# Performance work log

Measured on AMD Instinct MI355X. Metric: run time of the kernel, lower is better.

Reference implementation:

```python
import jax, jax.numpy as jnp
import numpy as np

N_ITER = 100
EPS = 1e-12


def _corr(x, k):
    # x: [C,H,W], k: [kh,kw]; per-channel 'same' cross-correlation, zero padding
    C = x.shape[0]
    kern = jnp.broadcast_to(k, (C, 1) + k.shape)
    return jax.lax.conv_general_dilated(
        x[None], kern, window_strides=(1, 1), padding='SAME',
        feature_group_count=C,
        dimension_numbers=('NCHW', 'OIHW', 'NCHW'))[0]


def _corr_t(x, k):
    # adjoint of zero-padded 'same' correlation = correlation with flipped kernel
    return _corr(x, k[::-1, ::-1])


def _A(x, kernel, reg_kernels, w2):
    # A x = K^T K x + sum_i w_i^2 R_i^T R_i x
    out = _corr_t(_corr(x, kernel), kernel)
    for i in range(reg_kernels.shape[0]):  # small fixed number of reg kernels
        rk = reg_kernels[i]
        out = out + w2[i] * _corr_t(_corr(x, rk), rk)
    return out


def setup_inputs() -> dict:
    key = jax.random.key(0)
    k1, k2, k3, k4 = jax.random.split(key, 4)
    image = jax.random.uniform(k1, (3, 768, 768), dtype=jnp.float32)
    kernel = jax.random.uniform(k2, (15, 15), dtype=jnp.float32)
    kernel = kernel / jnp.sum(kernel)  # normalized blur PSF
    reg_kernels = jax.random.normal(k3, (2, 5, 5), dtype=jnp.float32)
    reg_kernel_weights = jax.random.uniform(
        k4, (2,), dtype=jnp.float32, minval=1e-6, maxval=1.0)
    return {'image': image, 'kernel': kernel, 'reg_kernels': reg_kernels,
            'reg_kernel_weights': reg_kernel_weights}


def reference(image, kernel, reg_kernels, reg_kernel_weights):
    w2 = reg_kernel_weights ** 2
    # CG init: x0 = image, b = image, solve A x = K^T b
    KTb = _corr_t(image, kernel)
    r0 = KTb - _A(image, kernel, reg_kernels, w2)
    xrp0 = jnp.stack([image, r0, r0])  # [3, C, H, W]: x, r, p

    def body(xrp, _):
        x, r, p = xrp[0], xrp[1], xrp[2]
        Ap = _A(p, kernel, reg_kernels, w2)
        rtr = jnp.sum(r * r, axis=(1, 2), keepdims=True)      # per-channel [C,1,1]
        ptAp = jnp.sum(p * Ap, axis=(1, 2), keepdims=True)
        alpha = rtr / (ptAp + EPS)
        x_new = x + alpha * p
        r_new = r - alpha * Ap
        beta = jnp.sum(r_new * r_new, axis=(1, 2), keepdims=True) / (rtr + EPS)
        p_new = r_new + beta * p
        return jnp.stack([x_new, r_new, p_new]), None

    xrp, _ = jax.lax.scan(jax.checkpoint(body), xrp0, None, length=N_ITER)
    return xrp
```

## Files before the change

### kernel.cpp

```cpp
#include <hip/hip_runtime.h>

#define EPS 1e-12f

constexpr int H = 768, W = 768, C = 3;
constexpr int HW = H * W;
constexpr int CHW = C * HW;

constexpr int NSLOT = 16;
constexpr int SSTR = 16;
constexpr int SCALSZ = NSLOT * SSTR;

constexpr int SPW = 100, SPH = 60;
constexpr int S0W = 84,  S0H = 46;
constexpr int S1W = 76,  S1H = 36;
constexpr int UBUF = SPH * SPW;

__device__ __forceinline__ float block_reduce_256(float v, float* redbuf) {
    #pragma unroll
    for (int off = 32; off > 0; off >>= 1) v += __shfl_down(v, off, 64);
    const int tid = threadIdx.x;
    if ((tid & 63) == 0) redbuf[tid >> 6] = v;
    __syncthreads();
    return redbuf[0] + redbuf[1] + redbuf[2] + redbuf[3];
}

__device__ __forceinline__ float sum_slots(const float* base, int c) {
    float s = 0.f;
    #pragma unroll
    for (int k = 0; k < NSLOT; ++k) s += base[k * SSTR + c];
    return s;
}

__global__ void tap_prep_k(const float* __restrict__ k15, const float* __restrict__ rks,
                           float* __restrict__ taps) {
    const int tid = threadIdx.x;
    if (tid < 240) {
        const int i = tid >> 4, j = tid & 15;
        taps[tid]       = (j < 15) ? k15[i * 15 + j] : 0.f;
        taps[240 + tid] = (j < 15) ? k15[(14 - i) * 15 + (14 - j)] : 0.f;
    }
    if (tid < 80) {
        const int kk = tid / 40, rem = tid % 40, i = rem >> 3, j = rem & 7;
        taps[480 + tid] = (j < 5) ? rks[kk * 25 + i * 5 + j] : 0.f;
        taps[560 + tid] = (j < 5) ? rks[kk * 25 + (4 - i) * 5 + (4 - j)] : 0.f;
    }
}

template <int MODE>
__global__ __launch_bounds__(256) void fusedA_k(
    const float* __restrict__ in, const float* __restrict__ rvec,
    const float* __restrict__ taps, const float* __restrict__ rw,
    float* __restrict__ Ap, float* __restrict__ outR,
    float* __restrict__ outP, float* __restrict__ outX,
    const float* __restrict__ bnum, const float* __restrict__ bden,
    float* __restrict__ red)
{
    __shared__ __align__(16) float ub[UBUF];
    __shared__ __align__(16) float st1[S1H * S1W];
    __shared__ __align__(16) float st2[S1H * S1W];
    __shared__ float redbuf[4];

    const float* kt   = taps;
    const float* ktf  = taps + 240;
    const float* rkt  = taps + 480;
    const float* rktf = taps + 560;

    const int c = blockIdx.z;
    const int bx = blockIdx.x * 64, by = blockIdx.y * 32;
    const int tid = threadIdx.x;
    const float* inC = in + c * HW;

    float beta = 0.f;
    if (MODE == 2) beta = sum_slots(bnum, c) / (sum_slots(bden, c) + EPS);

    for (int t = tid; t < SPH * 96; t += 256) {
        const int ly = t / 96, lx = t - ly * 96;
        const int gy = by - 14 + ly, gx = bx - 14 + lx;
        float v = 0.f;
        if ((unsigned)gy < (unsigned)H && (unsigned)gx < (unsigned)W) {
            const int g = gy * W + gx;
            v = inC[g];
            if (MODE == 2) v = rvec[c * HW + g] + beta * v;
        }
        ub[ly * SPW + lx] = v;
    }
    __syncthreads();

    const int oy = tid >> 3;
    const int ox = (tid & 7) << 3;

    {
        const int s0 = tid, s1 = tid + 256;
        const int row0 = s0 / 9, c0 = (s0 - row0 * 9) << 3;
        const int row1 = s1 / 9, c1 = (s1 - row1 * 9) << 3;
        const bool v1 = (s1 < 324);
        float b0[8], c0a[8], b1[8], c1a[8];
        #pragma unroll
        for (int k = 0; k < 8; ++k) { b0[k] = 0.f; c0a[k] = 0.f; b1[k] = 0.f; c1a[k] = 0.f; }

        float4 kb0 = *(const float4*)(rkt + 0), kb1 = *(const float4*)(rkt + 4);
        float4 kc0 = *(const float4*)(rkt + 40), kc1 = *(const float4*)(rkt + 44);
        #pragma unroll 1
        for (int i = 0; i < 5; ++i) {
            const int ip = (i < 4) ? i + 1 : 4;
            float4 nb0 = *(const float4*)(rkt + ip * 8),      nb1 = *(const float4*)(rkt + ip * 8 + 4);
            float4 nc0 = *(const float4*)(rkt + 40 + ip * 8), nc1 = *(const float4*)(rkt + 40 + ip * 8 + 4);
            float kb[8], kc[8];
            *(float4*)(kb) = kb0; *(float4*)(kb + 4) = kb1;
            *(float4*)(kc) = kc0; *(float4*)(kc + 4) = kc1;

            {
                const float* rp = ub + (row0 + 10 + i) * SPW + c0 + 8;
                float seg[16];
                #pragma unroll
                for (int q = 0; q < 4; ++q) *(float4*)(seg + 4 * q) = *(const float4*)(rp + 4 * q);
                #pragma unroll
                for (int j = 0; j < 5; ++j)
                    #pragma unroll
                    for (int k = 0; k < 8; ++k) {
                        b0[k]  = fmaf(seg[j + k + 2], kb[j], b0[k]);
                        c0a[k] = fmaf(seg[j + k + 2], kc[j], c0a[k]);
                    }
            }
            if (v1) {
                const float* rp = ub + (row1 + 10 + i) * SPW + c1 + 8;
                float seg[16];
                #pragma unroll
                for (int q = 0; q < 4; ++q) *(float4*)(seg + 4 * q) = *(const float4*)(rp + 4 * q);
                #pragma unroll
                for (int j = 0; j < 5; ++j)
                    #pragma unroll
                    for (int k = 0; k < 8; ++k) {
                        b1[k]  = fmaf(seg[j + k + 2], kb[j], b1[k]);
                        c1a[k] = fmaf(seg[j + k + 2], kc[j], c1a[k]);
                    }
            }
            kb0 = nb0; kb1 = nb1; kc0 = nc0; kc1 = nc1;
        }
        {
            const int gy = by - 2 + row0, gxb = bx - 2 + c0;
            #pragma unroll
            for (int k = 0; k < 8; ++k) {
                const bool bad = ((unsigned)gy >= (unsigned)H) || ((unsigned)(gxb + k) >= (unsigned)W);
                if (bad) { b0[k] = 0.f; c0a[k] = 0.f; }
            }
            float* o1 = st1 + row0 * S1W + c0;
            float* o2 = st2 + row0 * S1W + c0;
            *(float4*)(o1)     = make_float4(b0[0], b0[1], b0[2], b0[3]);
            *(float4*)(o1 + 4) = make_float4(b0[4], b0[5], b0[6], b0[7]);
            *(float4*)(o2)     = make_float4(c0a[0], c0a[1], c0a[2], c0a[3]);
            *(float4*)(o2 + 4) = make_float4(c0a[4], c0a[5], c0a[6], c0a[7]);
        }
        if (v1) {
            const int gy = by - 2 + row1, gxb = bx - 2 + c1;
            #pragma unroll
            for (int k = 0; k < 8; ++k) {
                const bool bad = ((unsigned)gy >= (unsigned)H) || ((unsigned)(gxb + k) >= (unsigned)W);
                if (bad) { b1[k] = 0.f; c1a[k] = 0.f; }
            }
            float* o1 = st1 + row1 * S1W + c1;
            float* o2 = st2 + row1 * S1W + c1;
            *(float4*)(o1)     = make_float4(b1[0], b1[1], b1[2], b1[3]);
            *(float4*)(o1 + 4) = make_float4(b1[4], b1[5], b1[6], b1[7]);
            *(float4*)(o2)     = make_float4(c1a[0], c1a[1], c1a[2], c1a[3]);
            *(float4*)(o2 + 4) = make_float4(c1a[4], c1a[5], c1a[6], c1a[7]);
        }
    }

    float pctr[8];
    {
        const float* ctr = ub + (oy + 14) * SPW + ox + 14;
        #pragma unroll
        for (int k = 0; k < 8; ++k) pctr[k] = ctr[k];
    }

    float vimg[8];
    if (MODE == 0) {
        #pragma unroll
        for (int k = 0; k < 8; ++k) vimg[k] = 0.f;
        #pragma unroll 1
        for (int i = 0; i < 15; ++i) {
            const float* rowp = ub + (oy + 7 + i) * SPW + ox + 4;
            float seg[28];
            #pragma unroll
            for (int q = 0; q < 7; ++q) *(float4*)(seg + 4 * q) = *(const float4*)(rowp + 4 * q);
            float kv[16];
            #pragma unroll
            for (int q = 0; q < 4; ++q) *(float4*)(kv + 4 * q) = *(const float4*)(ktf + i * 16 + 4 * q);
            #pragma unroll
            for (int j = 0; j < 15; ++j)
                #pragma unroll
                for (int k = 0; k < 8; ++k) vimg[k] = fmaf(seg[j + k + 3], kv[j], vimg[k]);
        }
    }

    const int s0 = tid, s1 = tid + 256;
    const int row0 = s0 / 10, ca0 = (s0 - row0 * 10) << 3;
    const int row1 = s1 / 10, ca1 = (s1 - row1 * 10) << 3;
    const bool av1 = (s1 < 460);
    float a0[8], a1[8];
    #pragma unroll
    for (int k = 0; k < 8; ++k) { a0[k] = 0.f; a1[k] = 0.f; }
    {
        float4 k0 = *(const float4*)(kt + 0), k1 = *(const float4*)(kt + 4);
        float4 k2 = *(const float4*)(kt + 8), k3 = *(const float4*)(kt + 12);
        #pragma unroll 1
        for (int i = 0; i < 15; ++i) {
            const int ip = (i < 14) ? i + 1 : 14;
            float4 n0 = *(const float4*)(kt + ip * 16),     n1 = *(const float4*)(kt + ip * 16 + 4);
            float4 n2 = *(const float4*)(kt + ip * 16 + 8), n3 = *(const float4*)(kt + ip * 16 + 12);
            float kv[16];
            *(float4*)(kv) = k0; *(float4*)(kv + 4) = k1;
            *(float4*)(kv + 8) = k2; *(float4*)(kv + 12) = k3;
            {
                const float* rp = ub + (row0 + i) * SPW + ca0;
                float seg[24];
                #pragma unroll
                for (int q = 0; q < 6; ++q) *(float4*)(seg + 4 * q) = *(const float4*)(rp + 4 * q);
                #pragma unroll
                for (int j = 0; j < 15; ++j)
                    #pragma unroll
                    for (int k = 0; k < 8; ++k) a0[k] = fmaf(seg[j + k], kv[j], a0[k]);
            }
            if (av1) {
                const float* rp = ub + (row1 + i) * SPW + ca1;
                float seg[24];
                #pragma unroll
                for (int q = 0; q < 6; ++q) *(float4*)(seg + 4 * q) = *(const float4*)(rp + 4 * q);
                #pragma unroll
                for (int j = 0; j < 15; ++j)
                    #pragma unroll
                    for (int k = 0; k < 8; ++k) a1[k] = fmaf(seg[j + k], kv[j], a1[k]);
            }
            k0 = n0; k1 = n1; k2 = n2; k3 = n3;
        }
    }
    {
        const int gy = by - 7 + row0, gxb = bx - 7 + ca0;
        #pragma unroll
        for (int k = 0; k < 8; ++k)
            if (((unsigned)gy >= (unsigned)H) || ((unsigned)(gxb + k) >= (unsigned)W)) a0[k] = 0.f;
    }
    if (av1) {
        const int gy = by - 7 + row1, gxb = bx - 7 + ca1;
        #pragma unroll
        for (int k = 0; k < 8; ++k)
            if (((unsigned)gy >= (unsigned)H) || ((unsigned)(gxb + k) >= (unsigned)W)) a1[k] = 0.f;
    }

    __syncthreads();

    {
        float* o = ub + row0 * S0W + ca0;
        *(float4*)(o)     = make_float4(a0[0], a0[1], a0[2], a0[3]);
        *(float4*)(o + 4) = make_float4(a0[4], a0[5], a0[6], a0[7]);
    }
    if (av1) {
        float* o = ub + row1 * S0W + ca1;
        *(float4*)(o)     = make_float4(a1[0], a1[1], a1[2], a1[3]);
        *(float4*)(o + 4) = make_float4(a1[4], a1[5], a1[6], a1[7]);
    }
    __syncthreads();

    float acc[8];
    #pragma unroll
    for (int k = 0; k < 8; ++k) acc[k] = 0.f;
    {
        float4 k0 = *(const float4*)(ktf + 0), k1 = *(const float4*)(ktf + 4);
        float4 k2 = *(const float4*)(ktf + 8), k3 = *(const float4*)(ktf + 12);
        #pragma unroll 1
        for (int i = 0; i < 15; ++i) {
            const int ip = (i < 14) ? i + 1 : 14;
            float4 n0 = *(const float4*)(ktf + ip * 16),     n1 = *(const float4*)(ktf + ip * 16 + 4);
            float4 n2 = *(const float4*)(ktf + ip * 16 + 8), n3 = *(const float4*)(ktf + ip * 16 + 12);
            float kv[16];
            *(float4*)(kv) = k0; *(float4*)(kv + 4) = k1;
            *(float4*)(kv + 8) = k2; *(float4*)(kv + 12) = k3;
            const float* rp = ub + (oy + i) * S0W + ox;
            float seg[24];
            #pragma unroll
            for (int q = 0; q < 6; ++q) *(float4*)(seg + 4 * q) = *(const float4*)(rp + 4 * q);
            #pragma unroll
            for (int j = 0; j < 15; ++j)
                #pragma unroll
                for (int k = 0; k < 8; ++k) acc[k] = fmaf(seg[j + k], kv[j], acc[k]);
            k0 = n0; k1 = n1; k2 = n2; k3 = n3;
        }
    }

    float accB[8], accC[8];
    #pragma unroll
    for (int k = 0; k < 8; ++k) { accB[k] = 0.f; accC[k] = 0.f; }
    {
        float4 kb0 = *(const float4*)(rktf + 0), kb1 = *(const float4*)(rktf + 4);
        float4 kc0 = *(const float4*)(rktf + 40), kc1 = *(const float4*)(rktf + 44);
        #pragma unroll 1
        for (int i = 0; i < 5; ++i) {
            const int ip = (i < 4) ? i + 1 : 4;
            float4 nb0 = *(const float4*)(rktf + ip * 8),      nb1 = *(const float4*)(rktf + ip * 8 + 4);
            float4 nc0 = *(const float4*)(rktf + 40 + ip * 8), nc1 = *(const float4*)(rktf + 40 + ip * 8 + 4);
            float kb[8], kc[8];
            *(float4*)(kb) = kb0; *(float4*)(kb + 4) = kb1;
            *(float4*)(kc) = kc0; *(float4*)(kc + 4) = kc1;
            const float* r1p = st1 + (oy + i) * S1W + ox;
            const float* r2p = st2 + (oy + i) * S1W + ox;
            float sA[12], sB[12];
            #pragma unroll
            for (int q = 0; q < 3; ++q) *(float4*)(sA + 4 * q) = *(const float4*)(r1p + 4 * q);
            #pragma unroll
            for (int q = 0; q < 3; ++q) *(float4*)(sB + 4 * q) = *(const float4*)(r2p + 4 * q);
            #pragma unroll
            for (int j = 0; j < 5; ++j)
                #pragma unroll
                for (int k = 0; k < 8; ++k) {
                    accB[k] = fmaf(sA[j + k], kb[j], accB[k]);
                    accC[k] = fmaf(sB[j + k], kc[j], accC[k]);
                }
            kb0 = nb0; kb1 = nb1; kc0 = nc0; kc1 = nc1;
        }
    }

    const float w0 = rw[0], w1 = rw[1];
    const float w02 = w0 * w0, w12 = w1 * w1;
    float v[8];
    #pragma unroll
    for (int k = 0; k < 8; ++k) v[k] = acc[k] + w02 * accB[k] + w12 * accC[k];

    const int g = c * HW + (by + oy) * W + bx + ox;
    float local = 0.f;
    if (MODE == 0) {
        #pragma unroll
        for (int k = 0; k < 8; ++k) v[k] = vimg[k] - v[k];
        *(float4*)(outR + g)     = make_float4(v[0], v[1], v[2], v[3]);
        *(float4*)(outR + g + 4) = make_float4(v[4], v[5], v[6], v[7]);
        *(float4*)(outP + g)     = make_float4(v[0], v[1], v[2], v[3]);
        *(float4*)(outP + g + 4) = make_float4(v[4], v[5], v[6], v[7]);
        *(float4*)(outX + g)     = make_float4(pctr[0], pctr[1], pctr[2], pctr[3]);
        *(float4*)(outX + g + 4) = make_float4(pctr[4], pctr[5], pctr[6], pctr[7]);
        #pragma unroll
        for (int k = 0; k < 8; ++k) local += v[k] * v[k];
    } else {
        *(float4*)(Ap + g)     = make_float4(v[0], v[1], v[2], v[3]);
        *(float4*)(Ap + g + 4) = make_float4(v[4], v[5], v[6], v[7]);
        #pragma unroll
        for (int k = 0; k < 8; ++k) local += pctr[k] * v[k];
        if (MODE == 2) {
            *(float4*)(outP + g)     = make_float4(pctr[0], pctr[1], pctr[2], pctr[3]);
            *(float4*)(outP + g + 4) = make_float4(pctr[4], pctr[5], pctr[6], pctr[7]);
        }
    }
    const float tot = block_reduce_256(local, redbuf);
    if (tid == 0) {
        const int bid = blockIdx.y * gridDim.x + blockIdx.x;
        atomicAdd(red + (bid & (NSLOT - 1)) * SSTR + c, tot);
    }
}

__global__ __launch_bounds__(256) void cg_update_k(
    float* __restrict__ x, float* __restrict__ r,
    const float* __restrict__ Ap, const float* __restrict__ p,
    const float* __restrict__ rtr_cur, const float* __restrict__ ptap,
    float* __restrict__ rtr_next)
{
    __shared__ float redbuf[4];
    const int c = blockIdx.z;
    const float n = sum_slots(rtr_cur, c), d = sum_slots(ptap, c);
    const float alpha = n / (d + EPS);
    const int idx = c * HW + (blockIdx.x * 256 + threadIdx.x) * 8;
    float local = 0.f;
    #pragma unroll
    for (int h = 0; h < 2; ++h) {
        const int o = idx + 4 * h;
        float4 xv = *(float4*)(x + o);
        float4 rv = *(float4*)(r + o);
        const float4 pv = *(const float4*)(p + o);
        const float4 av = *(const float4*)(Ap + o);
        xv.x = fmaf(alpha, pv.x, xv.x); rv.x = fmaf(-alpha, av.x, rv.x);
        xv.y = fmaf(alpha, pv.y, xv.y); rv.y = fmaf(-alpha, av.y, rv.y);
        xv.z = fmaf(alpha, pv.z, xv.z); rv.z = fmaf(-alpha, av.z, rv.z);
        xv.w = fmaf(alpha, pv.w, xv.w); rv.w = fmaf(-alpha, av.w, rv.w);
        *(float4*)(x + o) = xv;
        *(float4*)(r + o) = rv;
        local += rv.x * rv.x + rv.y * rv.y + rv.z * rv.z + rv.w * rv.w;
    }
    const float tot = block_reduce_256(local, redbuf);
    if (threadIdx.x == 0)
        atomicAdd(rtr_next + ((int)blockIdx.x & (NSLOT - 1)) * SSTR + c, tot);
}

__global__ __launch_bounds__(256) void p_final_k(
    const float* __restrict__ r, const float* __restrict__ p99, float* __restrict__ pout,
    const float* __restrict__ num, const float* __restrict__ den)
{
    const int c = blockIdx.z;
    const float beta = sum_slots(num, c) / (sum_slots(den, c) + EPS);
    const int idx = c * HW + (blockIdx.x * 256 + threadIdx.x) * 8;
    #pragma unroll
    for (int h = 0; h < 2; ++h) {
        const int o = idx + 4 * h;
        const float4 rv = *(const float4*)(r + o);
        const float4 pv = *(const float4*)(p99 + o);
        *(float4*)(pout + o) = make_float4(
            fmaf(beta, pv.x, rv.x), fmaf(beta, pv.y, rv.y),
            fmaf(beta, pv.z, rv.z), fmaf(beta, pv.w, rv.w));
    }
}

extern "C" void kernel_launch(void* const* d_in, const int* in_sizes, int n_in,
                              void* d_out, int out_size, void* d_ws, size_t ws_size,
                              hipStream_t stream)
{
    const float* img = (const float*)d_in[0];
    const float* k15 = (const float*)d_in[1];
    const float* rks = (const float*)d_in[2];
    const float* rw  = (const float*)d_in[3];

    float* out = (float*)d_out;
    float* xs = out;
    float* rs = out + CHW;
    float* ps = out + 2 * CHW;

    float* ws   = (float*)d_ws;
    float* buf0 = ws;
    float* Ap   = buf0 + CHW;
    float* scal = Ap + CHW;
    float* rtr2 = scal;
    float* ptap = scal + 101 * SCALSZ;
    float* taps = scal + 201 * SCALSZ;

    hipMemsetAsync(scal, 0, (size_t)(101 + 100) * SCALSZ * sizeof(float), stream);
    tap_prep_k<<<1, 256, 0, stream>>>(k15, rks, taps);

    const dim3 gc(W / 64, H / 32, C), bc(256);
    const dim3 ge(HW / 2048, 1, C);

    fusedA_k<0><<<gc, bc, 0, stream>>>(img, nullptr, taps, rw,
                                       nullptr, rs, buf0, xs,
                                       nullptr, nullptr, rtr2);

    for (int i = 0; i < 100; ++i) {
        float* pin  = (i & 1) ? buf0 : ps;
        float* pcur = (i & 1) ? ps : buf0;
        if (i == 0) {
            fusedA_k<1><<<gc, bc, 0, stream>>>(buf0, nullptr, taps, rw,
                                               Ap, nullptr, nullptr, nullptr,
                                               nullptr, nullptr, ptap);
        } else {
            fusedA_k<2><<<gc, bc, 0, stream>>>(pin, rs, taps, rw,
                                               Ap, nullptr, pcur, nullptr,
                                               rtr2 + i * SCALSZ, rtr2 + (i - 1) * SCALSZ,
                                               ptap + i * SCALSZ);
        }
        cg_update_k<<<ge, bc, 0, stream>>>(xs, rs, Ap, pcur,
                                           rtr2 + i * SCALSZ, ptap + i * SCALSZ,
                                           rtr2 + (i + 1) * SCALSZ);
    }
    p_final_k<<<ge, bc, 0, stream>>>(rs, ps, ps, rtr2 + 100 * SCALSZ, rtr2 + 99 * SCALSZ);
}
```

Baseline: 9.897 ms.

## Collapse normal-equation operator into single 29x29 stencil for interior tiles

Precomputes the composed kernel K^T K + sum w_i^2 R_i^T R_i as one 29x29 autocorrelation stencil and applies it in a new interior kernel. The interior kernel does a single pass, so it avoids staging the intermediate correlation results in shared memory. Border tiles, where zero padding makes the composed stencil wrong, still use the original two-pass fused kernel, launched on a remapped 1-D edge grid. The 29x29 stencil costs about 841 FMAs per pixel, versus fewer for separate 15x15 and 5x5 passes, so the trade is more arithmetic for less shared-memory traffic and fewer syncs, plus an extra launch per iteration.

```diff
diff --git a/kernel.cpp b/kernel.cpp
--- a/kernel.cpp
+++ b/kernel.cpp
@@ -14,6 +14,8 @@
 constexpr int S0W = 84,  S0H = 46;
 constexpr int S1W = 76,  S1H = 36;
 constexpr int UBUF = SPH * SPW;
+
+constexpr int IPW = 92, IPH = 60;
 
 __device__ __forceinline__ float block_reduce_256(float v, float* redbuf) {
     #pragma unroll
@@ -32,7 +34,7 @@
 }
 
 __global__ void tap_prep_k(const float* __restrict__ k15, const float* __restrict__ rks,
-                           float* __restrict__ taps) {
+                           const float* __restrict__ rw, float* __restrict__ taps) {
     const int tid = threadIdx.x;
     if (tid < 240) {
         const int i = tid >> 4, j = tid & 15;
@@ -44,9 +46,135 @@
         taps[480 + tid] = (j < 5) ? rks[kk * 25 + i * 5 + j] : 0.f;
         taps[560 + tid] = (j < 5) ? rks[kk * 25 + (4 - i) * 5 + (4 - j)] : 0.f;
     }
-}
-
-template <int MODE>
+    const float w20 = rw[0] * rw[0], w21 = rw[1] * rw[1];
+    for (int t = tid; t < 29 * 36; t += 256) {
+        const int uy = t / 36, ux = t - uy * 36;
+        float s = 0.f;
+        if (ux < 29) {
+            const int dy = uy - 14, dx = ux - 14;
+            for (int sy = 0; sy < 15; ++sy) {
+                const int ty = sy + dy;
+                if ((unsigned)ty >= 15u) continue;
+                for (int sx = 0; sx < 15; ++sx) {
+                    const int tx = sx + dx;
+                    if ((unsigned)tx < 15u) s += k15[sy * 15 + sx] * k15[ty * 15 + tx];
+                }
+            }
+            if (dy >= -4 && dy <= 4 && dx >= -4 && dx <= 4) {
+                float q0 = 0.f, q1 = 0.f;
+                for (int sy = 0; sy < 5; ++sy) {
+                    const int ty = sy + dy;
+                    if ((unsigned)ty >= 5u) continue;
+                    for (int sx = 0; sx < 5; ++sx) {
+                        const int tx = sx + dx;
+                        if ((unsigned)tx >= 5u) continue;
+                        q0 += rks[sy * 5 + sx] * rks[ty * 5 + tx];
+                        q1 += rks[25 + sy * 5 + sx] * rks[25 + ty * 5 + tx];
+                    }
+                }
+                s += w20 * q0 + w21 * q1;
+            }
+        }
+        taps[640 + t] = s;
+    }
+}
+
+template <bool WRITEP>
+__global__ __launch_bounds__(256) void interiorA_k(
+    const float* __restrict__ pprev, const float* __restrict__ rvec,
+    const float* __restrict__ tk,
+    float* __restrict__ Ap, float* __restrict__ outP,
+    const float* __restrict__ bnum, const float* __restrict__ bden,
+    float* __restrict__ red)
+{
+    __shared__ __align__(16) float pe[IPH * IPW];
+    __shared__ float redbuf[4];
+    const int c = blockIdx.z;
+    const int bx = 64 + blockIdx.x * 64, by = 32 + blockIdx.y * 32;
+    const int tid = threadIdx.x;
+    const float beta = sum_slots(bnum, c) / (sum_slots(bden, c) + EPS);
+    const float* pC = pprev + c * HW;
+    const float* rC = rvec + c * HW;
+    const int gy0 = by - 14, gx0 = bx - 14;
+
+    for (int t = tid; t < IPH * IPW; t += 256) {
+        const int ly = t / IPW, lx = t - ly * IPW;
+        const int g = (gy0 + ly) * W + gx0 + lx;
+        pe[t] = fmaf(beta, pC[g], rC[g]);
+    }
+    __syncthreads();
+
+    const int ox = (tid & 15) << 2;
+    const int o0 = (tid >> 4) << 1;
+
+    float a0[4], a1[4];
+    #pragma unroll
+    for (int k = 0; k < 4; ++k) { a0[k] = 0.f; a1[k] = 0.f; }
+
+    {
+        const float* rp = pe + o0 * IPW + ox;
+        float seg[32];
+        #pragma unroll
+        for (int q = 0; q < 8; ++q) *(float4*)(seg + 4 * q) = *(const float4*)(rp + 4 * q);
+        #pragma unroll
+        for (int j = 0; j < 29; ++j) {
+            const float kv = tk[j];
+            #pragma unroll
+            for (int k = 0; k < 4; ++k) a0[k] = fmaf(seg[j + k], kv, a0[k]);
+        }
+    }
+    #pragma unroll 1
+    for (int d = 1; d <= 28; ++d) {
+        const float* rp = pe + (o0 + d) * IPW + ox;
+        float seg[32];
+        #pragma unroll
+        for (int q = 0; q < 8; ++q) *(float4*)(seg + 4 * q) = *(const float4*)(rp + 4 * q);
+        const float* kr0 = tk + d * 36;
+        const float* kr1 = kr0 - 36;
+        #pragma unroll
+        for (int j = 0; j < 29; ++j) {
+            const float kv0 = kr0[j], kv1 = kr1[j];
+            #pragma unroll
+            for (int k = 0; k < 4; ++k) {
+                a0[k] = fmaf(seg[j + k], kv0, a0[k]);
+                a1[k] = fmaf(seg[j + k], kv1, a1[k]);
+            }
+        }
+    }
+    {
+        const float* rp = pe + (o0 + 29) * IPW + ox;
+        float seg[32];
+        #pragma unroll
+        for (int q = 0; q < 8; ++q) *(float4*)(seg + 4 * q) = *(const float4*)(rp + 4 * q);
+        const float* kr1 = tk + 28 * 36;
+        #pragma unroll
+        for (int j = 0; j < 29; ++j) {
+            const float kv = kr1[j];
+            #pragma unroll
+            for (int k = 0; k < 4; ++k) a1[k] = fmaf(seg[j + k], kv, a1[k]);
+        }
+    }
+
+    const int gbase = c * HW + (by + o0) * W + bx + ox;
+    const float* c0p = pe + (o0 + 14) * IPW + ox + 14;
+    const float* c1p = c0p + IPW;
+    *(float4*)(Ap + gbase)     = make_float4(a0[0], a0[1], a0[2], a0[3]);
+    *(float4*)(Ap + gbase + W) = make_float4(a1[0], a1[1], a1[2], a1[3]);
+    float local = 0.f;
+    #pragma unroll
+    for (int k = 0; k < 4; ++k) local += c0p[k] * a0[k] + c1p[k] * a1[k];
+    if (WRITEP) {
+        *(float4*)(outP + gbase)     = make_float4(c0p[0], c0p[1], c0p[2], c0p[3]);
+        *(float4*)(outP + gbase + W) = make_float4(c1p[0], c1p[1], c1p[2], c1p[3]);
+    }
+    const float tot = block_reduce_256(local, redbuf);
+    if (tid == 0) {
+        const int bid = blockIdx.y * gridDim.x + blockIdx.x;
+        atomicAdd(red + (bid & (NSLOT - 1)) * SSTR + c, tot);
+    }
+}
+
+template <int MODE, bool REMAP>
 __global__ __launch_bounds__(256) void fusedA_k(
     const float* __restrict__ in, const float* __restrict__ rvec,
     const float* __restrict__ taps, const float* __restrict__ rw,
@@ -65,8 +193,17 @@
     const float* rkt  = taps + 480;
     const float* rktf = taps + 560;
 
+    int tbx, tby;
+    if (REMAP) {
+        const int e = blockIdx.x;
+        if (e < 12)      { tbx = e;      tby = 0; }
+        else if (e < 24) { tbx = e - 12; tby = 23; }
+        else if (e < 46) { tbx = 0;      tby = 1 + (e - 24); }
+        else             { tbx = 11;     tby = 1 + (e - 46); }
+    } else { tbx = blockIdx.x; tby = blockIdx.y; }
+
     const int c = blockIdx.z;
-    const int bx = blockIdx.x * 64, by = blockIdx.y * 32;
+    const int bx = tbx * 64, by = tby * 32;
     const int tid = threadIdx.x;
     const float* inC = in + c * HW;
 
@@ -108,7 +245,6 @@
             float kb[8], kc[8];
             *(float4*)(kb) = kb0; *(float4*)(kb + 4) = kb1;
             *(float4*)(kc) = kc0; *(float4*)(kc + 4) = kc1;
-
             {
                 const float* rp = ub + (row0 + 10 + i) * SPW + c0 + 8;
                 float seg[16];
@@ -351,7 +487,7 @@
     }
     const float tot = block_reduce_256(local, redbuf);
     if (tid == 0) {
-        const int bid = blockIdx.y * gridDim.x + blockIdx.x;
+        const int bid = REMAP ? (int)blockIdx.x : (int)(blockIdx.y * gridDim.x + blockIdx.x);
         atomicAdd(red + (bid & (NSLOT - 1)) * SSTR + c, tot);
     }
 }
@@ -426,30 +562,39 @@
     float* scal = Ap + CHW;
     float* rtr2 = scal;
     float* ptap = scal + 101 * SCALSZ;
-    float* taps = scal + 201 * SCALSZ;
-
-    hipMemsetAsync(scal, 0, (size_t)(101 + 100) * SCALSZ * sizeof(float), stream);
-    tap_prep_k<<<1, 256, 0, stream>>>(k15, rks, taps);
-
-    const dim3 gc(W / 64, H / 32, C), bc(256);
+    float* zslot = scal + 201 * SCALSZ;
+    float* taps = scal + 202 * SCALSZ;
+
+    hipMemsetAsync(scal, 0, (size_t)202 * SCALSZ * sizeof(float), stream);
+    tap_prep_k<<<1, 256, 0, stream>>>(k15, rks, rw, taps);
+    const float* tk = taps + 640;
+
+    const dim3 gfull(12, 24, 3), bc(256);
+    const dim3 gint(10, 22, 3), gedge(68, 1, 3);
     const dim3 ge(HW / 2048, 1, C);
 
-    fusedA_k<0><<<gc, bc, 0, stream>>>(img, nullptr, taps, rw,
-                                       nullptr, rs, buf0, xs,
-                                       nullptr, nullptr, rtr2);
+    fusedA_k<0, false><<<gfull, bc, 0, stream>>>(img, nullptr, taps, rw,
+                                                 nullptr, rs, buf0, xs,
+                                                 nullptr, nullptr, rtr2);
 
     for (int i = 0; i < 100; ++i) {
         float* pin  = (i & 1) ? buf0 : ps;
         float* pcur = (i & 1) ? ps : buf0;
         if (i == 0) {
-            fusedA_k<1><<<gc, bc, 0, stream>>>(buf0, nullptr, taps, rw,
-                                               Ap, nullptr, nullptr, nullptr,
-                                               nullptr, nullptr, ptap);
+            interiorA_k<false><<<gint, bc, 0, stream>>>(buf0, buf0, tk,
+                                                        Ap, nullptr, zslot, zslot, ptap);
+            fusedA_k<1, true><<<gedge, bc, 0, stream>>>(buf0, nullptr, taps, rw,
+                                                        Ap, nullptr, nullptr, nullptr,
+                                                        nullptr, nullptr, ptap);
         } else {
-            fusedA_k<2><<<gc, bc, 0, stream>>>(pin, rs, taps, rw,
-                                               Ap, nullptr, pcur, nullptr,
-                                               rtr2 + i * SCALSZ, rtr2 + (i - 1) * SCALSZ,
-                                               ptap + i * SCALSZ);
+            interiorA_k<true><<<gint, bc, 0, stream>>>(pin, rs, tk,
+                                                       Ap, pcur,
+                                                       rtr2 + i * SCALSZ, rtr2 + (i - 1) * SCALSZ,
+                                                       ptap + i * SCALSZ);
+            fusedA_k<2, true><<<gedge, bc, 0, stream>>>(pin, rs, taps, rw,
+                                                        Ap, nullptr, pcur, nullptr,
+                                                        rtr2 + i * SCALSZ, rtr2 + (i - 1) * SCALSZ,
+                                                        ptap + i * SCALSZ);
         }
         cg_update_k<<<ge, bc, 0, stream>>>(xs, rs, Ap, pcur,
                                            rtr2 + i * SCALSZ, ptap + i * SCALSZ,
```

Measured after the change: 9.706 ms. No clear change (-1.9%).
